# Kernel optimization log

Measured on AMD Instinct MI355X. Metric: run time of the kernel, lower is better.

Reference implementation:

```python
import jax, jax.numpy as jnp
import numpy as np

N = 20000
F_IN = 128
HID = 128
HEADS = 8
NCLS = 18
NEG_SLOPE = 0.2


def setup_inputs() -> dict:
    key = jax.random.key(0)
    ks = jax.random.split(key, 12)
    x = jax.random.normal(ks[0], (N, F_IN), dtype=jnp.float32)
    edge_index = jax.random.randint(ks[1], (2, 200000), 0, N)
    sc1 = 1.0 / np.sqrt(F_IN)
    sc2 = 1.0 / np.sqrt(HEADS * HID)
    W1 = jax.random.normal(ks[2], (F_IN, HEADS * HID), dtype=jnp.float32) * sc1
    a1_src = jax.random.normal(ks[3], (HEADS, HID), dtype=jnp.float32) * sc1
    a1_dst = jax.random.normal(ks[4], (HEADS, HID), dtype=jnp.float32) * sc1
    b1 = jnp.zeros((HEADS * HID,), dtype=jnp.float32)
    W2 = jax.random.normal(ks[5], (HEADS * HID, NCLS), dtype=jnp.float32) * sc2
    a2_src = jax.random.normal(ks[6], (1, NCLS), dtype=jnp.float32) * sc2
    a2_dst = jax.random.normal(ks[7], (1, NCLS), dtype=jnp.float32) * sc2
    b2 = jnp.zeros((NCLS,), dtype=jnp.float32)
    return {"x": x, "edge_index": edge_index, "W1": W1, "a1_src": a1_src,
            "a1_dst": a1_dst, "b1": b1, "W2": W2, "a2_src": a2_src,
            "a2_dst": a2_dst, "b2": b2}


def gat_conv(x, src, dst, W, a_src, a_dst, b, heads, out_ch):
    n = x.shape[0]
    h = (x @ W).reshape(n, heads, out_ch)              # [N,H,C]
    alpha_s = jnp.sum(h * a_src, axis=-1)              # [N,H]
    alpha_d = jnp.sum(h * a_dst, axis=-1)              # [N,H]
    e = jax.nn.leaky_relu(alpha_s[src] + alpha_d[dst], NEG_SLOPE)  # [E,H]
    # per-destination softmax (segment softmax)
    m = jax.ops.segment_max(e, dst, num_segments=n)
    e = jnp.exp(e - m[dst])
    z = jax.ops.segment_sum(e, dst, num_segments=n)
    alpha = e / (z[dst] + 1e-16)                       # [E,H]
    out = jax.ops.segment_sum(alpha[:, :, None] * h[src], dst, num_segments=n)
    return out.reshape(n, heads * out_ch) + b


def reference(x, edge_index, W1, a1_src, a1_dst, b1, W2, a2_src, a2_dst, b2):
    n = x.shape[0]
    # PyG GATConv adds self-loops by default
    loops = jnp.arange(n, dtype=edge_index.dtype)
    src = jnp.concatenate([edge_index[0], loops])
    dst = jnp.concatenate([edge_index[1], loops])
    h = gat_conv(x, src, dst, W1, a1_src, a1_dst, b1, HEADS, HID)
    h = jax.nn.relu(h)
    # F.dropout(training=self.training) is identity in eval mode
    out = gat_conv(h, src, dst, W2, a2_src, a2_dst, b2, 1, NCLS)
    return out
```

## Files before the change

kernel.cpp:

```cpp
#include <hip/hip_runtime.h>
#include <math.h>

#define FIN 128
#define NH 8
#define HC 128
#define HD (NH*HC)
#define NC 18
#define NW2 32
#define NEG 0.2f

typedef __attribute__((ext_vector_type(8))) short bf16x8;
typedef __attribute__((ext_vector_type(4))) float f32x4;

__device__ __forceinline__ float lrelu(float v){ return v > 0.f ? v : NEG*v; }

__device__ __forceinline__ unsigned short f2b(float f){
  unsigned u = __float_as_uint(f);
  unsigned r = (u + 0x7fffu + ((u >> 16) & 1u)) >> 16;
  return (unsigned short)r;
}
__device__ __forceinline__ float b2f_lo(unsigned u){ return __uint_as_float(u << 16); }
__device__ __forceinline__ float b2f_hi(unsigned u){ return __uint_as_float(u & 0xffff0000u); }

__device__ __forceinline__ void acc8(float* a, float w, uint4 r){
  a[0] += w*b2f_lo(r.x); a[1] += w*b2f_hi(r.x);
  a[2] += w*b2f_lo(r.y); a[3] += w*b2f_hi(r.y);
  a[4] += w*b2f_lo(r.z); a[5] += w*b2f_hi(r.z);
  a[6] += w*b2f_lo(r.w); a[7] += w*b2f_hi(r.w);
}

__global__ __launch_bounds__(1024) void scan_k(const int* __restrict__ deg, int N,
                                               int* __restrict__ off, int* __restrict__ cursor){
  __shared__ int wsum[16];
  int t = threadIdx.x, lane = t & 63, wid = t >> 6;
  int PER = (N + 1023) >> 10;
  int base = t * PER;
  int sum = 0;
  for (int i = 0; i < PER; ++i) {
    int idx = base + i;
    if (idx < N) sum += deg[idx];
  }
  int x = sum;
  #pragma unroll
  for (int o = 1; o < 64; o <<= 1) {
    int y = __shfl_up(x, o, 64);
    if (lane >= o) x += y;
  }
  if (lane == 63) wsum[wid] = x;
  __syncthreads();
  if (wid == 0 && lane < 16) {
    int wv = wsum[lane];
    #pragma unroll
    for (int o = 1; o < 16; o <<= 1) {
      int y = __shfl_up(wv, o, 16);
      if (lane >= o) wv += y;
    }
    wsum[lane] = wv;
  }
  __syncthreads();
  int carry = x - sum + (wid > 0 ? wsum[wid-1] : 0);
  int run = carry;
  for (int i = 0; i < PER; ++i) {
    int idx = base + i;
    if (idx < N) {
      off[idx] = run; cursor[idx] = run;
      run += deg[idx];
    }
  }
  if (base < N && base + PER >= N) off[N] = run;
}

__global__ void scatter_k(const int* __restrict__ ei, int E0, int N,
                          int* __restrict__ cursor, int* __restrict__ csr){
  int e = blockIdx.x*256 + threadIdx.x;
  int tot = E0 + N;
  if (e >= tot) return;
  int src, dst;
  if (e < E0) { src = ei[e]; dst = ei[E0 + e]; }
  else        { src = e - E0; dst = src; }
  int p = atomicAdd(&cursor[dst], 1);
  csr[p] = src;
}

__global__ __launch_bounds__(256) void prep_k(const float* __restrict__ x,
    const float* __restrict__ W1, const float* __restrict__ W2,
    const float* __restrict__ a1s, const float* __restrict__ a1d,
    const int* __restrict__ ei,
    unsigned short* __restrict__ xb, unsigned short* __restrict__ w1t,
    unsigned short* __restrict__ w2t, unsigned short* __restrict__ ut_g,
    int* __restrict__ deg,
    int total8, int bX, int E0, int N){
  __shared__ unsigned short sT[FIN][64+2];
  int b = blockIdx.x, t = threadIdx.x;
  if (b < bX) {
    int i = b*256 + t;
    if (i < total8) {
      const float4* p = (const float4*)x + (size_t)i*2;
      float4 a = p[0], c = p[1];
      uint4 o;
      o.x = (unsigned)f2b(a.x) | ((unsigned)f2b(a.y) << 16);
      o.y = (unsigned)f2b(a.z) | ((unsigned)f2b(a.w) << 16);
      o.z = (unsigned)f2b(c.x) | ((unsigned)f2b(c.y) << 16);
      o.w = (unsigned)f2b(c.z) | ((unsigned)f2b(c.w) << 16);
      ((uint4*)xb)[i] = o;
    }
    return;
  }
  b -= bX;
  if (b < 16) {
    int n0 = b * 64;
    #pragma unroll
    for (int i = 0; i < 32; ++i) {
      int idx = i*256 + t;
      int k = idx >> 6, nl = idx & 63;
      sT[k][nl] = f2b(W1[(size_t)k*HD + n0 + nl]);
    }
    __syncthreads();
    #pragma unroll
    for (int i = 0; i < 16; ++i) {
      int nl = i*4 + (t >> 6);
      int kp = t & 63;
      unsigned u = (unsigned)sT[2*kp][nl] | ((unsigned)sT[2*kp+1][nl] << 16);
      *(unsigned*)&w1t[(size_t)(n0+nl)*FIN + 2*kp] = u;
    }
    return;
  }
  b -= 16;
  if (b < (NW2*HD)/256) {
    int idx = b*256 + t;
    int n = idx >> 10, k = idx & 1023;
    w2t[idx] = (n < NC) ? f2b(W2[(size_t)k*NC + n]) : (unsigned short)0;
    return;
  }
  b -= (NW2*HD)/256;
  if (b < 16) {
    int c = b;
    int h = c >> 1;
    const float* av = (c & 1) ? &a1d[h*HC] : &a1s[h*HC];
    if (t < FIN) {
      const float4* wr = (const float4*)&W1[(size_t)t*HD + h*HC];
      const float4* ap = (const float4*)av;
      float s = 0.f;
      #pragma unroll 8
      for (int q = 0; q < HC/4; ++q) {
        float4 w4 = wr[q], a4 = ap[q];
        s += w4.x*a4.x + w4.y*a4.y + w4.z*a4.z + w4.w*a4.w;
      }
      ut_g[c*FIN + t] = f2b(s);
    }
    return;
  }
  b -= 16;
  {
    int e = b*256 + t;
    int tot = E0 + N;
    if (e >= tot) return;
    int dst = (e < E0) ? ei[E0 + e] : (e - E0);
    atomicAdd(&deg[dst], 1);
  }
}

__global__ __launch_bounds__(256) void gemm1_mfma_k(const unsigned short* __restrict__ xb,
    const unsigned short* __restrict__ w1t, const unsigned short* __restrict__ ut_g,
    unsigned short* __restrict__ g1b, float* __restrict__ as1, float* __restrict__ ad1,
    int N){
  __shared__ unsigned short sA[128][136];
  __shared__ unsigned short sB[128][136];
  __shared__ unsigned short sU[16][136];
  int t = threadIdx.x, lane = t & 63, wid = t >> 6;
  int bm = blockIdx.x * 128;
  int head = blockIdx.y;
  int bn = head * 128;
  #pragma unroll
  for (int i = 0; i < 2; ++i) {
    int idx = i*256 + t;
    int row = idx >> 2, seg = idx & 3;
    int gm = bm + row;
    uint4 a0,a1,a2,a3;
    if (gm < N) {
      const uint4* gp = (const uint4*)(xb + (size_t)gm*FIN + seg*32);
      a0 = gp[0]; a1 = gp[1]; a2 = gp[2]; a3 = gp[3];
    } else {
      a0 = a1 = a2 = a3 = make_uint4(0,0,0,0);
    }
    uint4* lp = (uint4*)&sA[row][seg*32];
    lp[0]=a0; lp[1]=a1; lp[2]=a2; lp[3]=a3;
  }
  #pragma unroll
  for (int i = 0; i < 2; ++i) {
    int idx = i*256 + t;
    int row = idx >> 2, seg = idx & 3;
    const uint4* gp = (const uint4*)(w1t + (size_t)(bn + row)*FIN + seg*32);
    uint4* lp = (uint4*)&sB[row][seg*32];
    lp[0]=gp[0]; lp[1]=gp[1]; lp[2]=gp[2]; lp[3]=gp[3];
  }
  bool alpha_blk = (head == 0);
  if (alpha_blk) {
    int row = t >> 4, seg = t & 15;
    *(uint4*)&sU[row][seg*8] = *(const uint4*)&ut_g[row*FIN + seg*8];
  }
  __syncthreads();
  int wr = wid >> 1, wc = wid & 1;
  int lr = lane & 15, kb = lane >> 4;
  bool alpha_wave = alpha_blk && (wc == 0);
  f32x4 acc[4][4];
  f32x4 accA[4];
  #pragma unroll
  for (int mi = 0; mi < 4; ++mi) {
    f32x4 z = {0.f,0.f,0.f,0.f};
    accA[mi] = z;
    #pragma unroll
    for (int ni = 0; ni < 4; ++ni) acc[mi][ni] = z;
  }
  #pragma unroll
  for (int ks = 0; ks < 4; ++ks) {
    int ko = ks*32 + kb*8;
    bf16x8 a[4], b[4];
    #pragma unroll
    for (int mi = 0; mi < 4; ++mi)
      a[mi] = *(const bf16x8*)&sA[wr*64 + mi*16 + lr][ko];
    #pragma unroll
    for (int ni = 0; ni < 4; ++ni)
      b[ni] = *(const bf16x8*)&sB[wc*64 + ni*16 + lr][ko];
    #pragma unroll
    for (int mi = 0; mi < 4; ++mi)
      #pragma unroll
      for (int ni = 0; ni < 4; ++ni)
        acc[mi][ni] = __builtin_amdgcn_mfma_f32_16x16x32_bf16(a[mi], b[ni], acc[mi][ni], 0, 0, 0);
    if (alpha_wave) {
      bf16x8 ub = *(const bf16x8*)&sU[lr][ko];
      #pragma unroll
      for (int mi = 0; mi < 4; ++mi)
        accA[mi] = __builtin_amdgcn_mfma_f32_16x16x32_bf16(a[mi], ub, accA[mi], 0, 0, 0);
    }
  }
  __syncthreads();

  if (alpha_wave) {
    int hcol = lr >> 1;
    float* dst0 = (lr & 1) ? ad1 : as1;
    #pragma unroll
    for (int mi = 0; mi < 4; ++mi)
      #pragma unroll
      for (int r = 0; r < 4; ++r) {
        int row = bm + wr*64 + mi*16 + kb*4 + r;
        if (row < N) dst0[(size_t)row*NH + hcol] = accA[mi][r];
      }
  }
  #pragma unroll
  for (int mi = 0; mi < 4; ++mi)
    #pragma unroll
    for (int ni = 0; ni < 4; ++ni) {
      int col = wc*64 + ni*16 + lr;
      #pragma unroll
      for (int r = 0; r < 4; ++r)
        sA[wr*64 + mi*16 + kb*4 + r][col] = f2b(acc[mi][ni][r]);
    }
  __syncthreads();
  {
    int row = t >> 1, half = t & 1;
    int grow = bm + row;
    if (grow < N) {
      uint4* dst = (uint4*)(g1b + (size_t)grow*HD + bn + half*64);
      const uint4* src = (const uint4*)&sA[row][half*64];
      #pragma unroll
      for (int q = 0; q < 8; ++q) dst[q] = src[q];
    }
  }
}

__global__ __launch_bounds__(256) void attn1_k(const unsigned short* __restrict__ g1b,
    const float* __restrict__ as1, const float* __restrict__ ad1,
    const int* __restrict__ off, const int* __restrict__ csr,
    const float* __restrict__ b1, unsigned short* __restrict__ hb, int N){
  int t = threadIdx.x, lane = t & 63, wid = t >> 6;
  int d = blockIdx.x*4 + wid;
  if (d >= N) return;
  int beg = off[d], deg = off[d+1] - beg;
  int hg = lane >> 3;
  float adg = ad1[d*NH + hg];
  float m = -1e30f, z = 0.f;
  float acc[16];
  #pragma unroll
  for (int i = 0; i < 16; ++i) acc[i] = 0.f;

  int j = 0;
  for (; j + 4 <= deg; j += 4) {
    int s0 = csr[beg+j+0], s1 = csr[beg+j+1], s2 = csr[beg+j+2], s3 = csr[beg+j+3];
    const uint4* p0 = (const uint4*)(g1b + (size_t)s0*HD) + lane*2;
    const uint4* p1 = (const uint4*)(g1b + (size_t)s1*HD) + lane*2;
    const uint4* p2 = (const uint4*)(g1b + (size_t)s2*HD) + lane*2;
    const uint4* p3 = (const uint4*)(g1b + (size_t)s3*HD) + lane*2;
    uint4 r00 = p0[0], r01 = p0[1];
    uint4 r10 = p1[0], r11 = p1[1];
    uint4 r20 = p2[0], r21 = p2[1];
    uint4 r30 = p3[0], r31 = p3[1];
    float e0 = lrelu(as1[s0*NH+hg] + adg);
    float e1 = lrelu(as1[s1*NH+hg] + adg);
    float e2 = lrelu(as1[s2*NH+hg] + adg);
    float e3 = lrelu(as1[s3*NH+hg] + adg);
    float em = fmaxf(fmaxf(e0,e1), fmaxf(e2,e3));
    if (em > m) {
      float sc = __expf(m - em);
      z *= sc;
      #pragma unroll
      for (int i = 0; i < 16; ++i) acc[i] *= sc;
      m = em;
    }
    float w0 = __expf(e0 - m), w1 = __expf(e1 - m);
    float w2 = __expf(e2 - m), w3 = __expf(e3 - m);
    z += w0 + w1 + w2 + w3;
    acc8(acc, w0, r00); acc8(acc+8, w0, r01);
    acc8(acc, w1, r10); acc8(acc+8, w1, r11);
    acc8(acc, w2, r20); acc8(acc+8, w2, r21);
    acc8(acc, w3, r30); acc8(acc+8, w3, r31);
  }
  for (; j < deg; ++j) {
    int s = csr[beg+j];
    const uint4* p = (const uint4*)(g1b + (size_t)s*HD) + lane*2;
    uint4 r0 = p[0], r1 = p[1];
    float e = lrelu(as1[s*NH+hg] + adg);
    if (e > m) {
      float sc = __expf(m - e);
      z *= sc;
      #pragma unroll
      for (int i = 0; i < 16; ++i) acc[i] *= sc;
      m = e;
    }
    float w = __expf(e - m);
    z += w;
    acc8(acc, w, r0); acc8(acc+8, w, r1);
  }

  float zinv = 1.f / (z + 1e-16f);
  int cb = lane*16;
  uint o[8];
  #pragma unroll
  for (int q = 0; q < 4; ++q) {
    float4 bv = *(const float4*)&b1[cb + q*4];
    float v0 = fmaxf(acc[q*4+0]*zinv + bv.x, 0.f);
    float v1 = fmaxf(acc[q*4+1]*zinv + bv.y, 0.f);
    float v2 = fmaxf(acc[q*4+2]*zinv + bv.z, 0.f);
    float v3 = fmaxf(acc[q*4+3]*zinv + bv.w, 0.f);
    o[q*2+0] = (unsigned)f2b(v0) | ((unsigned)f2b(v1) << 16);
    o[q*2+1] = (unsigned)f2b(v2) | ((unsigned)f2b(v3) << 16);
  }
  uint4* dst = (uint4*)(hb + (size_t)d*HD) + lane*2;
  dst[0] = make_uint4(o[0], o[1], o[2], o[3]);
  dst[1] = make_uint4(o[4], o[5], o[6], o[7]);
}

__global__ __launch_bounds__(256) void gemm2_k(const unsigned short* __restrict__ hb,
    const unsigned short* __restrict__ w2t, const float* __restrict__ a2s_g, const float* __restrict__ a2d_g,
    float* __restrict__ g2, float* __restrict__ as2, float* __restrict__ ad2, int N){
  __shared__ float red[4][32][32];
  int t = threadIdx.x, lane = t & 63, wid = t >> 6;
  int bm = blockIdx.x * 32;
  int lr = lane & 15, kb = lane >> 4;
  int kw = wid * 256;
  f32x4 acc[2][2];
  #pragma unroll
  for (int mi = 0; mi < 2; ++mi)
    #pragma unroll
    for (int ni = 0; ni < 2; ++ni) {
      f32x4 z = {0.f,0.f,0.f,0.f};
      acc[mi][ni] = z;
    }
  bf16x8 zf;
  #pragma unroll
  for (int q = 0; q < 8; ++q) zf[q] = 0;
  int r0n = bm + lr, r1n = bm + 16 + lr;
  #pragma unroll
  for (int ks = 0; ks < 8; ++ks) {
    int k = kw + ks*32 + kb*8;
    bf16x8 a0 = (r0n < N) ? *(const bf16x8*)&hb[(size_t)r0n*HD + k] : zf;
    bf16x8 a1 = (r1n < N) ? *(const bf16x8*)&hb[(size_t)r1n*HD + k] : zf;
    bf16x8 b0 = *(const bf16x8*)&w2t[(size_t)lr*HD + k];
    bf16x8 b1 = *(const bf16x8*)&w2t[(size_t)(16+lr)*HD + k];
    acc[0][0] = __builtin_amdgcn_mfma_f32_16x16x32_bf16(a0, b0, acc[0][0], 0,0,0);
    acc[0][1] = __builtin_amdgcn_mfma_f32_16x16x32_bf16(a0, b1, acc[0][1], 0,0,0);
    acc[1][0] = __builtin_amdgcn_mfma_f32_16x16x32_bf16(a1, b0, acc[1][0], 0,0,0);
    acc[1][1] = __builtin_amdgcn_mfma_f32_16x16x32_bf16(a1, b1, acc[1][1], 0,0,0);
  }
  #pragma unroll
  for (int mi = 0; mi < 2; ++mi)
    #pragma unroll
    for (int ni = 0; ni < 2; ++ni)
      #pragma unroll
      for (int r = 0; r < 4; ++r)
        red[wid][mi*16 + kb*4 + r][ni*16 + lr] = acc[mi][ni][r];
  __syncthreads();
  int row = t >> 3;
  int c4 = (t & 7) * 4;
  float tot[4];
  #pragma unroll
  for (int q = 0; q < 4; ++q)
    tot[q] = red[0][row][c4+q] + red[1][row][c4+q] + red[2][row][c4+q] + red[3][row][c4+q];
  int n = bm + row;
  float ps = 0.f, pd = 0.f;
  #pragma unroll
  for (int q = 0; q < 4; ++q) {
    int c = c4 + q;
    if (c < NC) {
      ps += tot[q]*a2s_g[c];
      pd += tot[q]*a2d_g[c];
    }
  }
  #pragma unroll
  for (int o = 1; o < 8; o <<= 1) {
    ps += __shfl_xor(ps, o, 8);
    pd += __shfl_xor(pd, o, 8);
  }
  if (n < N) {
    #pragma unroll
    for (int q = 0; q < 4; ++q) {
      int c = c4 + q;
      if (c < NC) g2[(size_t)n*NC + c] = tot[q];
    }
    if ((t & 7) == 0) { as2[n] = ps; ad2[n] = pd; }
  }
}

__global__ __launch_bounds__(256) void attn2_k(const float* __restrict__ g2,
    const float* __restrict__ as2, const float* __restrict__ ad2,
    const int* __restrict__ off, const int* __restrict__ csr,
    const float* __restrict__ b2, float* __restrict__ out, int N){
  int t = threadIdx.x, lane = t & 63, wid = t >> 6;
  int d = blockIdx.x*4 + wid;
  if (d >= N) return;
  int beg = off[d], deg = off[d+1] - beg;
  float adv = ad2[d];
  int g = lane / 18;
  int c = lane - g*18;
  float m = -1e30f, z = 0.f, acc = 0.f;
  if (g < 3) {
    int j = g;
    for (; j + 3 < deg; j += 6) {
      int sa = csr[beg+j], sb = csr[beg+j+3];
      float va = g2[(size_t)sa*NC + c];
      float vb = g2[(size_t)sb*NC + c];
      float ea = lrelu(as2[sa] + adv);
      float eb = lrelu(as2[sb] + adv);
      float em = fmaxf(ea, eb);
      if (em > m) { float sc = __expf(m - em); z *= sc; acc *= sc; m = em; }
      float wa = __expf(ea - m), wb = __expf(eb - m);
      z += wa + wb;
      acc += wa*va + wb*vb;
    }
    for (; j < deg; j += 3) {
      int s = csr[beg+j];
      float v = g2[(size_t)s*NC + c];
      float e = lrelu(as2[s] + adv);
      if (e > m) { float sc = __expf(m - e); z *= sc; acc *= sc; m = e; }
      float w = __expf(e - m);
      z += w;
      acc += w*v;
    }
  }
  float m0 = __shfl(m, 0),  m1 = __shfl(m, 18), m2 = __shfl(m, 36);
  float M  = fmaxf(m0, fmaxf(m1, m2));
  float e0 = __expf(m0 - M), e1 = __expf(m1 - M), e2 = __expf(m2 - M);
  float z0 = __shfl(z, 0),  z1 = __shfl(z, 18), z2 = __shfl(z, 36);
  int cl = (lane < NC) ? lane : 0;
  float a0 = __shfl(acc, cl), a1 = __shfl(acc, cl+18), a2 = __shfl(acc, cl+36);
  if (lane < NC) {
    float Z = z0*e0 + z1*e1 + z2*e2;
    float A = a0*e0 + a1*e1 + a2*e2;
    out[(size_t)d*NC + lane] = A / (Z + 1e-16f) + b2[lane];
  }
}

extern "C" void kernel_launch(void* const* d_in, const int* in_sizes, int n_in,
                              void* d_out, int out_size, void* d_ws, size_t ws_size,
                              hipStream_t stream){
  const float* x   = (const float*)d_in[0];
  const int*   ei  = (const int*)d_in[1];
  const float* W1  = (const float*)d_in[2];
  const float* a1s = (const float*)d_in[3];
  const float* a1d = (const float*)d_in[4];
  const float* b1  = (const float*)d_in[5];
  const float* W2  = (const float*)d_in[6];
  const float* a2s = (const float*)d_in[7];
  const float* a2d = (const float*)d_in[8];
  const float* b2  = (const float*)d_in[9];
  float* out = (float*)d_out;
  int N  = in_sizes[0] / FIN;
  int E0 = in_sizes[1] / 2;
  int Etot = E0 + N;

  float* as1 = (float*)d_ws;
  float* ad1 = as1 + (size_t)N*NH;
  float* g2  = ad1 + (size_t)N*NH;
  float* as2 = g2 + (size_t)N*NC;
  float* ad2 = as2 + N;
  unsigned short* g1b = (unsigned short*)(ad2 + N);
  unsigned short* hb  = g1b + (size_t)N*HD;
  int* deg    = (int*)(hb + (size_t)N*HD);
  int* off    = deg + N;
  int* cursor = off + N + 4;
  int* csr    = cursor + N;
  unsigned short* w2t  = (unsigned short*)(csr + Etot);
  unsigned short* ut_g = w2t + (size_t)NW2*HD;
  unsigned short* xb  = hb;
  unsigned short* w1t = hb + (size_t)N*FIN;

  hipMemsetAsync(deg, 0, sizeof(int)*(size_t)N, stream);

  int total8 = N*FIN/8;
  int bX = (total8 + 255)/256;
  int bH = (Etot + 255)/256;
  int bW2 = (NW2*HD)/256;
  prep_k<<<bX + 16 + bW2 + 16 + bH, 256, 0, stream>>>(x, W1, W2, a1s, a1d, ei,
                                                      xb, w1t, w2t, ut_g, deg,
                                                      total8, bX, E0, N);
  scan_k<<<1, 1024, 0, stream>>>(deg, N, off, cursor);
  scatter_k<<<(Etot+255)/256, 256, 0, stream>>>(ei, E0, N, cursor, csr);

  dim3 g1grid((N+127)/128, HD/128);
  gemm1_mfma_k<<<g1grid, 256, 0, stream>>>(xb, w1t, ut_g, g1b, as1, ad1, N);
  attn1_k<<<(N+3)/4, 256, 0, stream>>>(g1b, as1, ad1, off, csr, b1, hb, N);
  gemm2_k<<<(N+31)/32, 256, 0, stream>>>(hb, w2t, a2s, a2d, g2, as2, ad2, N);
  attn2_k<<<(N+3)/4, 256, 0, stream>>>(g2, as2, ad2, off, csr, b2, out, N);
}
```

Baseline: 255.1 us.

## Fuse layer-2 projection GEMM into layer-1 attention epilogue

Measured after the change: 259.4 us. No clear change (+1.7%).

```diff
diff --git a/kernel.cpp b/kernel.cpp
--- a/kernel.cpp
+++ b/kernel.cpp
@@ -272,13 +272,21 @@
 __global__ __launch_bounds__(256) void attn1_k(const unsigned short* __restrict__ g1b,
     const float* __restrict__ as1, const float* __restrict__ ad1,
     const int* __restrict__ off, const int* __restrict__ csr,
-    const float* __restrict__ b1, unsigned short* __restrict__ hb, int N){
+    const float* __restrict__ b1, const unsigned short* __restrict__ w2t,
+    const float* __restrict__ a2s_g, const float* __restrict__ a2d_g,
+    float* __restrict__ g2, float* __restrict__ as2, float* __restrict__ ad2, int N){
+  __shared__ unsigned short tile[16][1032];
+  __shared__ float red[4][4][32];
   int t = threadIdx.x, lane = t & 63, wid = t >> 6;
   int d = blockIdx.x*4 + wid;
-  if (d >= N) return;
-  int beg = off[d], deg = off[d+1] - beg;
+  bool active = (d < N);
+  int beg = 0, deg = 0;
   int hg = lane >> 3;
-  float adg = ad1[d*NH + hg];
+  float adg = 0.f;
+  if (active) {
+    beg = off[d]; deg = off[d+1] - beg;
+    adg = ad1[d*NH + hg];
+  }
   float m = -1e30f, z = 0.f;
   float acc[16];
   #pragma unroll
@@ -332,92 +340,62 @@
     acc8(acc, w, r0); acc8(acc+8, w, r1);
   }
 
-  float zinv = 1.f / (z + 1e-16f);
-  int cb = lane*16;
-  uint o[8];
-  #pragma unroll
-  for (int q = 0; q < 4; ++q) {
-    float4 bv = *(const float4*)&b1[cb + q*4];
-    float v0 = fmaxf(acc[q*4+0]*zinv + bv.x, 0.f);
-    float v1 = fmaxf(acc[q*4+1]*zinv + bv.y, 0.f);
-    float v2 = fmaxf(acc[q*4+2]*zinv + bv.z, 0.f);
-    float v3 = fmaxf(acc[q*4+3]*zinv + bv.w, 0.f);
-    o[q*2+0] = (unsigned)f2b(v0) | ((unsigned)f2b(v1) << 16);
-    o[q*2+1] = (unsigned)f2b(v2) | ((unsigned)f2b(v3) << 16);
-  }
-  uint4* dst = (uint4*)(hb + (size_t)d*HD) + lane*2;
-  dst[0] = make_uint4(o[0], o[1], o[2], o[3]);
-  dst[1] = make_uint4(o[4], o[5], o[6], o[7]);
-}
-
-__global__ __launch_bounds__(256) void gemm2_k(const unsigned short* __restrict__ hb,
-    const unsigned short* __restrict__ w2t, const float* __restrict__ a2s_g, const float* __restrict__ a2d_g,
-    float* __restrict__ g2, float* __restrict__ as2, float* __restrict__ ad2, int N){
-  __shared__ float red[4][32][32];
-  int t = threadIdx.x, lane = t & 63, wid = t >> 6;
-  int bm = blockIdx.x * 32;
-  int lr = lane & 15, kb = lane >> 4;
-  int kw = wid * 256;
-  f32x4 acc[2][2];
-  #pragma unroll
-  for (int mi = 0; mi < 2; ++mi)
-    #pragma unroll
-    for (int ni = 0; ni < 2; ++ni) {
-      f32x4 z = {0.f,0.f,0.f,0.f};
-      acc[mi][ni] = z;
-    }
-  bf16x8 zf;
-  #pragma unroll
-  for (int q = 0; q < 8; ++q) zf[q] = 0;
-  int r0n = bm + lr, r1n = bm + 16 + lr;
-  #pragma unroll
-  for (int ks = 0; ks < 8; ++ks) {
-    int k = kw + ks*32 + kb*8;
-    bf16x8 a0 = (r0n < N) ? *(const bf16x8*)&hb[(size_t)r0n*HD + k] : zf;
-    bf16x8 a1 = (r1n < N) ? *(const bf16x8*)&hb[(size_t)r1n*HD + k] : zf;
-    bf16x8 b0 = *(const bf16x8*)&w2t[(size_t)lr*HD + k];
-    bf16x8 b1 = *(const bf16x8*)&w2t[(size_t)(16+lr)*HD + k];
-    acc[0][0] = __builtin_amdgcn_mfma_f32_16x16x32_bf16(a0, b0, acc[0][0], 0,0,0);
-    acc[0][1] = __builtin_amdgcn_mfma_f32_16x16x32_bf16(a0, b1, acc[0][1], 0,0,0);
-    acc[1][0] = __builtin_amdgcn_mfma_f32_16x16x32_bf16(a1, b0, acc[1][0], 0,0,0);
-    acc[1][1] = __builtin_amdgcn_mfma_f32_16x16x32_bf16(a1, b1, acc[1][1], 0,0,0);
-  }
-  #pragma unroll
-  for (int mi = 0; mi < 2; ++mi)
-    #pragma unroll
-    for (int ni = 0; ni < 2; ++ni)
-      #pragma unroll
-      for (int r = 0; r < 4; ++r)
-        red[wid][mi*16 + kb*4 + r][ni*16 + lr] = acc[mi][ni][r];
-  __syncthreads();
-  int row = t >> 3;
-  int c4 = (t & 7) * 4;
-  float tot[4];
-  #pragma unroll
-  for (int q = 0; q < 4; ++q)
-    tot[q] = red[0][row][c4+q] + red[1][row][c4+q] + red[2][row][c4+q] + red[3][row][c4+q];
-  int n = bm + row;
-  float ps = 0.f, pd = 0.f;
-  #pragma unroll
-  for (int q = 0; q < 4; ++q) {
-    int c = c4 + q;
-    if (c < NC) {
-      ps += tot[q]*a2s_g[c];
-      pd += tot[q]*a2d_g[c];
-    }
-  }
-  #pragma unroll
-  for (int o = 1; o < 8; o <<= 1) {
-    ps += __shfl_xor(ps, o, 8);
-    pd += __shfl_xor(pd, o, 8);
-  }
-  if (n < N) {
+  {
+    float zinv = 1.f / (z + 1e-16f);
+    int cb = lane*16;
+    uint o[8];
     #pragma unroll
     for (int q = 0; q < 4; ++q) {
-      int c = c4 + q;
-      if (c < NC) g2[(size_t)n*NC + c] = tot[q];
-    }
-    if ((t & 7) == 0) { as2[n] = ps; ad2[n] = pd; }
+      float4 bv = *(const float4*)&b1[cb + q*4];
+      float v0 = fmaxf(acc[q*4+0]*zinv + bv.x, 0.f);
+      float v1 = fmaxf(acc[q*4+1]*zinv + bv.y, 0.f);
+      float v2 = fmaxf(acc[q*4+2]*zinv + bv.z, 0.f);
+      float v3 = fmaxf(acc[q*4+3]*zinv + bv.w, 0.f);
+      o[q*2+0] = (unsigned)f2b(v0) | ((unsigned)f2b(v1) << 16);
+      o[q*2+1] = (unsigned)f2b(v2) | ((unsigned)f2b(v3) << 16);
+    }
+    uint4* lp = (uint4*)&tile[wid][lane*16];
+    lp[0] = make_uint4(o[0], o[1], o[2], o[3]);
+    lp[1] = make_uint4(o[4], o[5], o[6], o[7]);
+  }
+  __syncthreads();
+
+  {
+    int lr = lane & 15, kb = lane >> 4;
+    f32x4 c0 = {0.f,0.f,0.f,0.f}, c1 = {0.f,0.f,0.f,0.f};
+    #pragma unroll
+    for (int ks = 0; ks < 8; ++ks) {
+      int k = wid*256 + ks*32 + kb*8;
+      bf16x8 af = *(const bf16x8*)&tile[lr][k];
+      bf16x8 b0 = *(const bf16x8*)&w2t[(size_t)lr*HD + k];
+      bf16x8 b1f = *(const bf16x8*)&w2t[(size_t)(16+lr)*HD + k];
+      c0 = __builtin_amdgcn_mfma_f32_16x16x32_bf16(af, b0, c0, 0,0,0);
+      c1 = __builtin_amdgcn_mfma_f32_16x16x32_bf16(af, b1f, c1, 0,0,0);
+    }
+    if (kb == 0) {
+      #pragma unroll
+      for (int r = 0; r < 4; ++r) {
+        red[wid][r][lr]      = c0[r];
+        red[wid][r][16 + lr] = c1[r];
+      }
+    }
+  }
+  __syncthreads();
+  if (t < 128) {
+    int dl = t >> 5, c = t & 31;
+    float v = red[0][dl][c] + red[1][dl][c] + red[2][dl][c] + red[3][dl][c];
+    float vs = (c < NC) ? v * a2s_g[c] : 0.f;
+    float vd = (c < NC) ? v * a2d_g[c] : 0.f;
+    #pragma unroll
+    for (int o = 1; o < 32; o <<= 1) {
+      vs += __shfl_xor(vs, o, 32);
+      vd += __shfl_xor(vd, o, 32);
+    }
+    int dg = blockIdx.x*4 + dl;
+    if (dg < N) {
+      if (c < NC) g2[(size_t)dg*NC + c] = v;
+      if (c == 0) { as2[dg] = vs; ad2[dg] = vd; }
+    }
   }
 }
 
@@ -493,16 +471,16 @@
   float* g2  = ad1 + (size_t)N*NH;
   float* as2 = g2 + (size_t)N*NC;
   float* ad2 = as2 + N;
-  unsigned short* g1b = (unsigned short*)(ad2 + N);
-  unsigned short* hb  = g1b + (size_t)N*HD;
-  int* deg    = (int*)(hb + (size_t)N*HD);
+  unsigned short* g1b  = (unsigned short*)(ad2 + N);
+  unsigned short* scr  = g1b + (size_t)N*HD;
+  int* deg    = (int*)(scr + (size_t)N*HD);
   int* off    = deg + N;
   int* cursor = off + N + 4;
   int* csr    = cursor + N;
   unsigned short* w2t  = (unsigned short*)(csr + Etot);
   unsigned short* ut_g = w2t + (size_t)NW2*HD;
-  unsigned short* xb  = hb;
-  unsigned short* w1t = hb + (size_t)N*FIN;
+  unsigned short* xb  = scr;
+  unsigned short* w1t = scr + (size_t)N*FIN;
 
   hipMemsetAsync(deg, 0, sizeof(int)*(size_t)N, stream);
 
@@ -518,7 +496,7 @@
 
   dim3 g1grid((N+127)/128, HD/128);
   gemm1_mfma_k<<<g1grid, 256, 0, stream>>>(xb, w1t, ut_g, g1b, as1, ad1, N);
-  attn1_k<<<(N+3)/4, 256, 0, stream>>>(g1b, as1, ad1, off, csr, b1, hb, N);
-  gemm2_k<<<(N+31)/32, 256, 0, stream>>>(hb, w2t, a2s, a2d, g2, as2, ad2, N);
+  attn1_k<<<(N+3)/4, 256, 0, stream>>>(g1b, as1, ad1, off, csr, b1, w2t,
+                                       a2s, a2d, g2, as2, ad2, N);
   attn2_k<<<(N+3)/4, 256, 0, stream>>>(g2, as2, ad2, off, csr, b2, out, N);
 }
```
